# Kernel optimization log

Hardware: AMD Instinct MI355X
Metric: run time of the kernel (lower is better)

The kernel has to match this reference:

```python
import jax, jax.numpy as jnp
import numpy as np

N_NODES = 50000
N_EDGES = 800000
D_IN = 16


def gcn_conv(x, edge_index, W, b, n_nodes):
    """PyG GCNConv: x' = D^{-1/2} (A + I) D^{-1/2} X W + b (add_self_loops=True)."""
    h = x @ W  # [N, d_out] - transform before propagate (small d => cheaper)
    src = jnp.concatenate([edge_index[0], jnp.arange(n_nodes)])  # add self-loops
    dst = jnp.concatenate([edge_index[1], jnp.arange(n_nodes)])
    deg = jax.ops.segment_sum(jnp.ones_like(dst, dtype=h.dtype), dst,
                              num_segments=n_nodes)  # in-degree incl. self-loop
    deg_inv_sqrt = jnp.where(deg > 0, jax.lax.rsqrt(deg), 0.0)
    norm = deg_inv_sqrt[src] * deg_inv_sqrt[dst]  # [E+N]
    msg = h[src] * norm[:, None]                  # gather + scale
    out = jax.ops.segment_sum(msg, dst, num_segments=n_nodes)  # scatter-add
    return out + b


def setup_inputs() -> dict:
    key = jax.random.key(0)
    ks = jax.random.split(key, 16)
    d = D_IN
    x = jax.random.normal(ks[0], (N_NODES, d), dtype=jnp.float32)
    edge_index = jax.random.randint(ks[1], (2, N_EDGES), 0, N_NODES, dtype=jnp.int64)

    def glorot(k, fan_in, fan_out):
        s = (6.0 / (fan_in + fan_out)) ** 0.5
        return jax.random.uniform(k, (fan_in, fan_out), jnp.float32, -s, s)

    return {
        "x": x,
        "edge_index": edge_index,
        "W1": glorot(ks[2], d, 2 * d),      "b1": jnp.zeros((2 * d,), jnp.float32),
        "W2": glorot(ks[3], 2 * d, 4 * d),  "b2": jnp.zeros((4 * d,), jnp.float32),
        "W3": glorot(ks[4], 4 * d, 8 * d),  "b3": jnp.zeros((8 * d,), jnp.float32),
        "Wl1": glorot(ks[5], 8 * d, 4 * d), "bl1": jnp.zeros((4 * d,), jnp.float32),
        "Wl2": glorot(ks[6], 4 * d, 2 * d), "bl2": jnp.zeros((2 * d,), jnp.float32),
        "Wl3": glorot(ks[7], 2 * d, d),     "bl3": jnp.zeros((d,), jnp.float32),
    }


def reference(x, edge_index, W1, b1, W2, b2, W3, b3, Wl1, bl1, Wl2, bl2, Wl3, bl3):
    n = x.shape[0]
    # note: original applies relu twice per conv; relu is idempotent
    out = jax.nn.relu(gcn_conv(x, edge_index, W1, b1, n))
    out = jax.nn.relu(gcn_conv(out, edge_index, W2, b2, n))
    out = jax.nn.relu(gcn_conv(out, edge_index, W3, b3, n))
    out = jax.nn.relu(out @ Wl1 + bl1)
    out = jax.nn.relu(out @ Wl2 + bl2)
    out = jax.nn.relu(out @ Wl3 + bl3)
    return out
```

## Files before the change

kernel.cpp:

```cpp
#include <hip/hip_runtime.h>

#define TPB 256
#define TE  2048
#define MAXB 6144

typedef _Float16 half_t;
typedef _Float16 half4 __attribute__((ext_vector_type(4)));
typedef _Float16 half8 __attribute__((ext_vector_type(8)));
typedef float float8v __attribute__((ext_vector_type(8)));

static inline int cdiv(int a, int b) { return (a + b - 1) / b; }


__global__ void k_zero_int(int* p, int n) {
    int i = blockIdx.x * blockDim.x + threadIdx.x;
    if (i < n) p[i] = 0;
}

__global__ void __launch_bounds__(TPB)
k_binscatter(const int* __restrict__ src, const int* __restrict__ dst,
             int* __restrict__ bcur, unsigned int* __restrict__ gbuf,
             int e, int nb) {
    __shared__ int lcnt[256], loffs[256], lcur[256], gres[256];
    __shared__ int ss[256];
    __shared__ unsigned int ldata[TE];
    const int tid = threadIdx.x;
    const int base = blockIdx.x * TE;
    const int cnt = min(TE, e - base);
    lcnt[tid] = 0;
    __syncthreads();

    unsigned int myv[TE / TPB];
    int myb[TE / TPB];
#pragma unroll
    for (int k = 0; k < TE / TPB; ++k) {
        int j = tid + k * TPB;
        if (j < cnt) {
            int d = dst[base + j], s = src[base + j];
            int b = d >> 8;
            myv[k] = ((unsigned)b << 24) | ((unsigned)(d & 255) << 16) | (unsigned)s;
            myb[k] = b;
            atomicAdd(&lcnt[b], 1);
        } else myb[k] = -1;
    }
    __syncthreads();
    {
        int v = lcnt[tid];
        ss[tid] = v;
        __syncthreads();
        for (int d = 1; d < 256; d <<= 1) {
            int x2 = (tid >= d) ? ss[tid - d] : 0;
            __syncthreads();
            ss[tid] += x2;
            __syncthreads();
        }
        loffs[tid] = ss[tid] - v;
        lcur[tid] = ss[tid] - v;
    }
    __syncthreads();
    if (tid < nb && lcnt[tid])
        gres[tid] = tid * MAXB + atomicAdd(&bcur[tid], lcnt[tid]);
#pragma unroll
    for (int k = 0; k < TE / TPB; ++k) {
        if (myb[k] >= 0) {
            int p = atomicAdd(&lcur[myb[k]], 1);
            ldata[p] = myv[k];
        }
    }
    __syncthreads();
    for (int j = tid; j < cnt; j += TPB) {
        unsigned int v = ldata[j];
        int b = v >> 24;
        gbuf[gres[b] + (j - loffs[b])] = v & 0xFFFFFFu;
    }
}

__global__ void __launch_bounds__(TPB)
k_csr(const unsigned int* __restrict__ gbuf, const int* __restrict__ bcur,
      const float* __restrict__ x, int* __restrict__ offs,
      unsigned short* __restrict__ nch, float* __restrict__ dinv,
      unsigned short* __restrict__ ssrc, half_t* __restrict__ G, int n, int nb) {
    __shared__ int ss[256], cnt[256], loffs2[256], lcur2[256], pcnt[256];
    __shared__ float sdinv[256];
    __shared__ unsigned short stage[MAXB];
    const int b = blockIdx.x;
    const int t = threadIdx.x;
    const int s0 = b * MAXB;
    const int m = bcur[b];

    cnt[t] = 0;
    __syncthreads();
    for (int j = t; j < m; j += TPB)
        atomicAdd(&cnt[(gbuf[s0 + j] >> 16) & 255], 1);
    __syncthreads();
    {
        int v = cnt[t];
        int pv = (v + 7) & ~7;
        pcnt[t] = pv;
        ss[t] = pv;
        __syncthreads();
        for (int d = 1; d < 256; d <<= 1) {
            int x2 = (t >= d) ? ss[t - d] : 0;
            __syncthreads();
            ss[t] += x2;
            __syncthreads();
        }
        loffs2[t] = ss[t] - pv;
        lcur2[t] = ss[t] - pv;
        float di = rsqrtf((float)v + 1.0f);
        sdinv[t] = di;
        int node = b * 256 + t;
        if (node < n) {
            offs[node] = s0 + loffs2[t];
            nch[node] = (unsigned short)(pv >> 3);
            dinv[node] = di;
        }
    }
    __syncthreads();
    for (int j = t; j < m; j += TPB) {
        unsigned int v = gbuf[s0 + j];
        int p = atomicAdd(&lcur2[(v >> 16) & 255], 1);
        stage[p] = (unsigned short)(v & 0xFFFFu);
    }
    __syncthreads();
    {
        int base2 = loffs2[t] + cnt[t], end2 = loffs2[t] + pcnt[t];
        for (int q = base2; q < end2; ++q) stage[q] = (unsigned short)n;
    }
    __syncthreads();
    const int tot = ss[255];
    for (int j = t; j < tot; j += TPB) ssrc[s0 + j] = stage[j];

    const int base = b * 256;
    const int cn = min(256, n - base);
    const float4* X4 = (const float4*)x;
    half4* G4 = (half4*)G;
    for (int j = t; j < cn * 4; j += TPB) {
        int nl = j >> 2, k4 = j & 3;
        float4 v = X4[(size_t)(base + nl) * 4 + k4];
        float d = sdinv[nl];
        half4 h;
        h.x = (half_t)(v.x * d); h.y = (half_t)(v.y * d);
        h.z = (half_t)(v.z * d); h.w = (half_t)(v.w * d);
        G4[(size_t)(base + nl) * 4 + k4] = h;
    }
    if (b == 0 && t < 4) G4[(size_t)n * 4 + t] = half4{0, 0, 0, 0};
}

template<int DI, int DO, int R, bool SCALE, bool OUT_HALF, bool WHALF, bool ZSENT>
__global__ void __launch_bounds__(TPB, 4)
k_conv(const int* __restrict__ offs, const unsigned short* __restrict__ nch,
       const unsigned short* __restrict__ ssrc,
       const half_t* __restrict__ G, const float* __restrict__ dinv,
       const float* __restrict__ W, const float* __restrict__ b,
       void* __restrict__ outp, int n) {
    constexpr int CT = DO / 4;
    constexpr int RT = TPB / CT;
    constexpr int TM = RT * R;
    constexpr int K4 = DI / 4;
    constexpr int PX = K4 + 1;
    constexpr int C  = DI / 8;
    static_assert(TM * C == TPB, "gather/gemm tile mismatch");
    __shared__ float4 sW4[WHALF ? 1 : DI * CT];
    __shared__ half4  sWh[WHALF ? DI * CT : 1];
    __shared__ float4 sX4[TM * PX];
    __shared__ int soffs[TM];
    __shared__ unsigned short snch[TM];
    const int tid = threadIdx.x;
    const int r0 = blockIdx.x * TM;

    const float4* Wg = (const float4*)W;
    for (int t = tid; t < DI * CT; t += TPB) {
        float4 w = Wg[t];
        if (WHALF) {
            half4 h;
            h.x = (half_t)w.x; h.y = (half_t)w.y;
            h.z = (half_t)w.z; h.w = (half_t)w.w;
            sWh[t] = h;
        } else {
            sW4[t] = w;
        }
    }
    if (tid < TM) {
        int row = r0 + tid;
        soffs[tid] = (row < n) ? offs[row] : 0;
        snch[tid] = (row < n) ? nch[row] : (unsigned short)0;
    }
    __syncthreads();

    {
        int lrow = tid / C;
        int gc = tid - lrow * C;
        int row = r0 + lrow;
        float8v acc;
#pragma unroll
        for (int q = 0; q < 8; ++q) acc[q] = 0.f;
        if (row < n) {
            const half8* Grow = (const half8*)G;
            const unsigned gcU = (unsigned)gc;
            half8 hs = Grow[(unsigned)row * C + gcU];
#pragma unroll
            for (int q = 0; q < 8; ++q) acc[q] = (float)hs[q];
            const int nchunks = snch[lrow];
            const uint4* sv = (const uint4*)(ssrc + soffs[lrow]);
            int k = 0;
            for (; k + 2 <= nchunks; k += 2) {
                uint4 pa = sv[k];
                uint4 pb = sv[k + 1];
                unsigned a0 = pa.x & 0xFFFFu, a1 = pa.x >> 16;
                unsigned a2 = pa.y & 0xFFFFu, a3 = pa.y >> 16;
                unsigned a4 = pa.z & 0xFFFFu, a5 = pa.z >> 16;
                unsigned a6 = pa.w & 0xFFFFu, a7 = pa.w >> 16;
                unsigned b0 = pb.x & 0xFFFFu, b1 = pb.x >> 16;
                unsigned b2 = pb.y & 0xFFFFu, b3 = pb.y >> 16;
                unsigned b4 = pb.z & 0xFFFFu, b5 = pb.z >> 16;
                unsigned b6 = pb.w & 0xFFFFu, b7 = pb.w >> 16;
                half8 ga0 = Grow[a0 * C + gcU];
                half8 ga1 = Grow[a1 * C + gcU];
                half8 ga2 = Grow[a2 * C + gcU];
                half8 ga3 = Grow[a3 * C + gcU];
                half8 ga4 = Grow[a4 * C + gcU];
                half8 ga5 = Grow[a5 * C + gcU];
                half8 ga6 = Grow[a6 * C + gcU];
                half8 ga7 = Grow[a7 * C + gcU];
                half8 gb0 = Grow[b0 * C + gcU];
                half8 gb1 = Grow[b1 * C + gcU];
                half8 gb2 = Grow[b2 * C + gcU];
                half8 gb3 = Grow[b3 * C + gcU];
                half8 gb4 = Grow[b4 * C + gcU];
                half8 gb5 = Grow[b5 * C + gcU];
                half8 gb6 = Grow[b6 * C + gcU];
                half8 gb7 = Grow[b7 * C + gcU];
#pragma unroll
                for (int q = 0; q < 8; ++q)
                    acc[q] += (((((float)ga0[q] + (float)ga1[q]) + ((float)ga2[q] + (float)ga3[q]))
                             +  (((float)ga4[q] + (float)ga5[q]) + ((float)ga6[q] + (float)ga7[q])))
                             + ((((float)gb0[q] + (float)gb1[q]) + ((float)gb2[q] + (float)gb3[q]))
                             +  (((float)gb4[q] + (float)gb5[q]) + ((float)gb6[q] + (float)gb7[q]))));
            }
            if (k < nchunks) {
                uint4 pk = sv[k];
                unsigned a0 = pk.x & 0xFFFFu, a1 = pk.x >> 16;
                unsigned a2 = pk.y & 0xFFFFu, a3 = pk.y >> 16;
                unsigned a4 = pk.z & 0xFFFFu, a5 = pk.z >> 16;
                unsigned a6 = pk.w & 0xFFFFu, a7 = pk.w >> 16;
                half8 g0 = Grow[a0 * C + gcU];
                half8 g1 = Grow[a1 * C + gcU];
                half8 g2 = Grow[a2 * C + gcU];
                half8 g3 = Grow[a3 * C + gcU];
                half8 g4 = Grow[a4 * C + gcU];
                half8 g5 = Grow[a5 * C + gcU];
                half8 g6 = Grow[a6 * C + gcU];
                half8 g7 = Grow[a7 * C + gcU];
#pragma unroll
                for (int q = 0; q < 8; ++q)
                    acc[q] += (((float)g0[q] + (float)g1[q]) + ((float)g2[q] + (float)g3[q]))
                            + (((float)g4[q] + (float)g5[q]) + ((float)g6[q] + (float)g7[q]));
            }
            float di = dinv[row];
#pragma unroll
            for (int q = 0; q < 8; ++q) acc[q] *= di;
        }
        sX4[lrow * PX + 2 * gc]     = make_float4(acc[0], acc[1], acc[2], acc[3]);
        sX4[lrow * PX + 2 * gc + 1] = make_float4(acc[4], acc[5], acc[6], acc[7]);
    }
    __syncthreads();

    const int c = tid & (CT - 1);
    const int rg = tid / CT;
    const int rbase = rg * R;
    float4 acc[R];
#pragma unroll
    for (int r = 0; r < R; ++r) acc[r] = make_float4(0.f, 0.f, 0.f, 0.f);

#pragma unroll 2
    for (int k4 = 0; k4 < K4; ++k4) {
        float4 xv[R];
#pragma unroll
        for (int r = 0; r < R; ++r) xv[r] = sX4[(rbase + r) * PX + k4];
#pragma unroll
        for (int kk = 0; kk < 4; ++kk) {
            float4 wv;
            if (WHALF) {
                half4 wh = sWh[(k4 * 4 + kk) * CT + c];
                wv = make_float4((float)wh.x, (float)wh.y, (float)wh.z, (float)wh.w);
            } else {
                wv = sW4[(k4 * 4 + kk) * CT + c];
            }
#pragma unroll
            for (int r = 0; r < R; ++r) {
                float xs = (kk == 0) ? xv[r].x : (kk == 1) ? xv[r].y
                         : (kk == 2) ? xv[r].z : xv[r].w;
                acc[r].x += xs * wv.x; acc[r].y += xs * wv.y;
                acc[r].z += xs * wv.z; acc[r].w += xs * wv.w;
            }
        }
    }

    float4 bc = ((const float4*)b)[c];
#pragma unroll
    for (int r = 0; r < R; ++r) {
        int row = r0 + rbase + r;
        if (row < n) {
            float4 o;
            o.x = fmaxf(acc[r].x + bc.x, 0.f);
            o.y = fmaxf(acc[r].y + bc.y, 0.f);
            o.z = fmaxf(acc[r].z + bc.z, 0.f);
            o.w = fmaxf(acc[r].w + bc.w, 0.f);
            if (SCALE) {
                float d = dinv[row];
                o.x *= d; o.y *= d; o.z *= d; o.w *= d;
            }
            if (OUT_HALF) {
                half4 h;
                h.x = (half_t)o.x; h.y = (half_t)o.y;
                h.z = (half_t)o.z; h.w = (half_t)o.w;
                ((half4*)outp)[(size_t)row * CT + c] = h;
            } else {
                ((float4*)outp)[(size_t)row * CT + c] = o;
            }
        }
    }
    if (ZSENT && OUT_HALF && blockIdx.x == 0 && tid < CT)
        ((half4*)outp)[(size_t)n * CT + tid] = half4{0, 0, 0, 0};
}

__global__ void __launch_bounds__(256, 3)
k_head(const half_t* __restrict__ X,
       const float* __restrict__ W1, const float* __restrict__ b1,
       const float* __restrict__ W2, const float* __restrict__ b2,
       const float* __restrict__ W3, const float* __restrict__ b3,
       float* __restrict__ out, int n) {
    __shared__ half_t hW1[128 * 64];
    __shared__ half_t hW2[64 * 32];
    __shared__ half_t hW3[32 * 16];
    __shared__ float h1[64 * 65];
    __shared__ float h2[64 * 33];
    const int tid = threadIdx.x;
    const int r0 = blockIdx.x * 64;

    for (int t = tid; t < 128 * 64; t += 256) hW1[t] = (half_t)W1[t];
    for (int t = tid; t < 64 * 32; t += 256) hW2[t] = (half_t)W2[t];
    for (int t = tid; t < 32 * 16; t += 256) hW3[t] = (half_t)W3[t];
    __syncthreads();

    {
        const int c4 = tid & 15;
        const int rowg = tid >> 4;
        const half8* Xr = (const half8*)X;
        float acc[4][4];
#pragma unroll
        for (int r = 0; r < 4; ++r)
#pragma unroll
            for (int j = 0; j < 4; ++j) acc[r][j] = 0.f;
        for (int k8 = 0; k8 < 16; ++k8) {
            half8 xh[4];
#pragma unroll
            for (int r = 0; r < 4; ++r) {
                int row = r0 + rowg * 4 + r;
                if (row < n) xh[r] = Xr[(size_t)row * 16 + k8];
                else { half8 z; for (int q = 0; q < 8; ++q) z[q] = (half_t)0.f; xh[r] = z; }
            }
#pragma unroll
            for (int q = 0; q < 8; ++q) {
                int k = k8 * 8 + q;
                half4 w = *(const half4*)&hW1[k * 64 + c4 * 4];
                float w0 = (float)w.x, w1 = (float)w.y, w2 = (float)w.z, w3 = (float)w.w;
#pragma unroll
                for (int r = 0; r < 4; ++r) {
                    float xs = (float)xh[r][q];
                    acc[r][0] += xs * w0; acc[r][1] += xs * w1;
                    acc[r][2] += xs * w2; acc[r][3] += xs * w3;
                }
            }
        }
        float4 bc = ((const float4*)b1)[c4];
#pragma unroll
        for (int r = 0; r < 4; ++r) {
            int rl = rowg * 4 + r;
            h1[rl * 65 + c4 * 4 + 0] = fmaxf(acc[r][0] + bc.x, 0.f);
            h1[rl * 65 + c4 * 4 + 1] = fmaxf(acc[r][1] + bc.y, 0.f);
            h1[rl * 65 + c4 * 4 + 2] = fmaxf(acc[r][2] + bc.z, 0.f);
            h1[rl * 65 + c4 * 4 + 3] = fmaxf(acc[r][3] + bc.w, 0.f);
        }
    }
    __syncthreads();

    {
        const int c4 = tid & 7;
        const int rowg = tid >> 3;
        float acc[2][4];
#pragma unroll
        for (int r = 0; r < 2; ++r)
#pragma unroll
            for (int j = 0; j < 4; ++j) acc[r][j] = 0.f;
#pragma unroll 4
        for (int k = 0; k < 64; ++k) {
            half4 w = *(const half4*)&hW2[k * 32 + c4 * 4];
            float w0 = (float)w.x, w1 = (float)w.y, w2 = (float)w.z, w3 = (float)w.w;
#pragma unroll
            for (int r = 0; r < 2; ++r) {
                float xs = h1[(rowg * 2 + r) * 65 + k];
                acc[r][0] += xs * w0; acc[r][1] += xs * w1;
                acc[r][2] += xs * w2; acc[r][3] += xs * w3;
            }
        }
        float4 bc = ((const float4*)b2)[c4];
#pragma unroll
        for (int r = 0; r < 2; ++r) {
            int rl = rowg * 2 + r;
            h2[rl * 33 + c4 * 4 + 0] = fmaxf(acc[r][0] + bc.x, 0.f);
            h2[rl * 33 + c4 * 4 + 1] = fmaxf(acc[r][1] + bc.y, 0.f);
            h2[rl * 33 + c4 * 4 + 2] = fmaxf(acc[r][2] + bc.z, 0.f);
            h2[rl * 33 + c4 * 4 + 3] = fmaxf(acc[r][3] + bc.w, 0.f);
        }
    }
    __syncthreads();

    {
        const int c4 = tid & 3;
        const int rl = tid >> 2;
        float a0 = 0.f, a1 = 0.f, a2 = 0.f, a3 = 0.f;
#pragma unroll 4
        for (int k = 0; k < 32; ++k) {
            half4 w = *(const half4*)&hW3[k * 16 + c4 * 4];
            float xs = h2[rl * 33 + k];
            a0 += xs * (float)w.x; a1 += xs * (float)w.y;
            a2 += xs * (float)w.z; a3 += xs * (float)w.w;
        }
        int row = r0 + rl;
        if (row < n) {
            float4 bc = ((const float4*)b3)[c4];
            float4 o;
            o.x = fmaxf(a0 + bc.x, 0.f);
            o.y = fmaxf(a1 + bc.y, 0.f);
            o.z = fmaxf(a2 + bc.z, 0.f);
            o.w = fmaxf(a3 + bc.w, 0.f);
            ((float4*)out)[(size_t)row * 4 + c4] = o;
        }
    }
}

extern "C" void kernel_launch(void* const* d_in, const int* in_sizes, int n_in,
                              void* d_out, int out_size, void* d_ws, size_t ws_size,
                              hipStream_t stream) {
    const float* x   = (const float*)d_in[0];
    const int*   ei  = (const int*)d_in[1];
    const float* W1  = (const float*)d_in[2];
    const float* bb1 = (const float*)d_in[3];
    const float* W2  = (const float*)d_in[4];
    const float* bb2 = (const float*)d_in[5];
    const float* W3  = (const float*)d_in[6];
    const float* bb3 = (const float*)d_in[7];
    const float* Wl1 = (const float*)d_in[8];
    const float* bl1 = (const float*)d_in[9];
    const float* Wl2 = (const float*)d_in[10];
    const float* bl2 = (const float*)d_in[11];
    const float* Wl3 = (const float*)d_in[12];
    const float* bl3 = (const float*)d_in[13];
    float* out = (float*)d_out;

    const int n = in_sizes[0] / 16;
    const int e = in_sizes[1] / 2;
    const int* src = ei;
    const int* dst = ei + e;
    const int nb = cdiv(n, 256);

    char* p = (char*)d_ws;
    auto alloc = [&](size_t bytes) {
        char* r = p;
        p += (bytes + 255) & ~(size_t)255;
        return r;
    };
    float*          dinv = (float*)         alloc((size_t)n * 4);
    int*            offs = (int*)           alloc((size_t)n * 4);
    unsigned short* nch  = (unsigned short*)alloc((size_t)n * 2);
    int*            bcur = (int*)           alloc(256 * 4);
    unsigned int*   gbuf = (unsigned int*)  alloc((size_t)nb * MAXB * 4);
    unsigned short* ssrc = (unsigned short*)alloc((size_t)nb * MAXB * 2);
    half_t*         H1   = (half_t*)        alloc((size_t)(n + 1) * 64 * 2);
    half_t*         H2   = (half_t*)        alloc((size_t)(n + 1) * 32 * 2);
    half_t*         X3h  = (half_t*)        alloc((size_t)n * 128 * 2);

    k_zero_int<<<1, 256, 0, stream>>>(bcur, 256);
    k_binscatter<<<cdiv(e, TE), TPB, 0, stream>>>(src, dst, bcur, gbuf, e, nb);
    k_csr<<<nb, TPB, 0, stream>>>(gbuf, bcur, x, offs, nch, dinv, ssrc, H1, n, nb);

    k_conv<16, 32, 4, true, true, false, true><<<cdiv(n, 128), TPB, 0, stream>>>(
        offs, nch, ssrc, H1, dinv, W1, bb1, H2, n);
    k_conv<32, 64, 4, true, true, false, true><<<cdiv(n, 64), TPB, 0, stream>>>(
        offs, nch, ssrc, H2, dinv, W2, bb2, H1, n);
    k_conv<64, 128, 4, false, true, true, false><<<cdiv(n, 32), TPB, 0, stream>>>(
        offs, nch, ssrc, H1, dinv, W3, bb3, X3h, n);

    k_head<<<cdiv(n, 64), 256, 0, stream>>>(X3h, Wl1, bl1, Wl2, bl2, Wl3, bl3, out, n);
}
```

Baseline: 198.9 us.

## Fuse third GCN conv with MLP head and count node degrees during binning

The third graph convolution is merged with the three-layer MLP head into one kernel. The 128-wide hidden features now stay in shared memory, through a union that reuses the conv-stage buffers, so the fp16 X3 intermediate is no longer written to and read back from global memory. Per-node in-degrees are counted with global atomics in the binning kernel, which removes the counting pass over gbuf in the CSR kernel. A single memset replaces the zeroing kernel. In exchange, every edge now issues a global atomic, and the head converts Wl1 to fp16 in every 32-row block, which adds per-block weight-load overhead.

Result: slower. 218.2 us (+9.7%).

```diff
diff --git a/kernel.cpp b/kernel.cpp
--- a/kernel.cpp
+++ b/kernel.cpp
@@ -12,15 +12,10 @@
 static inline int cdiv(int a, int b) { return (a + b - 1) / b; }
 
 
-__global__ void k_zero_int(int* p, int n) {
-    int i = blockIdx.x * blockDim.x + threadIdx.x;
-    if (i < n) p[i] = 0;
-}
-
 __global__ void __launch_bounds__(TPB)
 k_binscatter(const int* __restrict__ src, const int* __restrict__ dst,
-             int* __restrict__ bcur, unsigned int* __restrict__ gbuf,
-             int e, int nb) {
+             int* __restrict__ bcur, int* __restrict__ ncnt,
+             unsigned int* __restrict__ gbuf, int e, int nb) {
     __shared__ int lcnt[256], loffs[256], lcur[256], gres[256];
     __shared__ int ss[256];
     __shared__ unsigned int ldata[TE];
@@ -41,6 +36,7 @@
             myv[k] = ((unsigned)b << 24) | ((unsigned)(d & 255) << 16) | (unsigned)s;
             myb[k] = b;
             atomicAdd(&lcnt[b], 1);
+            atomicAdd(&ncnt[d], 1);
         } else myb[k] = -1;
     }
     __syncthreads();
@@ -77,10 +73,11 @@
 
 __global__ void __launch_bounds__(TPB)
 k_csr(const unsigned int* __restrict__ gbuf, const int* __restrict__ bcur,
-      const float* __restrict__ x, int* __restrict__ offs,
-      unsigned short* __restrict__ nch, float* __restrict__ dinv,
-      unsigned short* __restrict__ ssrc, half_t* __restrict__ G, int n, int nb) {
-    __shared__ int ss[256], cnt[256], loffs2[256], lcur2[256], pcnt[256];
+      const int* __restrict__ ncnt, const float* __restrict__ x,
+      int* __restrict__ offs, unsigned short* __restrict__ nch,
+      float* __restrict__ dinv, unsigned short* __restrict__ ssrc,
+      half_t* __restrict__ G, int n, int nb) {
+    __shared__ int ss[256], lcur2[256];
     __shared__ float sdinv[256];
     __shared__ unsigned short stage[MAXB];
     const int b = blockIdx.x;
@@ -88,45 +85,35 @@
     const int s0 = b * MAXB;
     const int m = bcur[b];
 
-    cnt[t] = 0;
-    __syncthreads();
-    for (int j = t; j < m; j += TPB)
-        atomicAdd(&cnt[(gbuf[s0 + j] >> 16) & 255], 1);
-    __syncthreads();
-    {
-        int v = cnt[t];
-        int pv = (v + 7) & ~7;
-        pcnt[t] = pv;
-        ss[t] = pv;
+    const int v = ncnt[b * 256 + t];
+    const int pv = (v + 7) & ~7;
+    ss[t] = pv;
+    __syncthreads();
+    for (int d = 1; d < 256; d <<= 1) {
+        int x2 = (t >= d) ? ss[t - d] : 0;
         __syncthreads();
-        for (int d = 1; d < 256; d <<= 1) {
-            int x2 = (t >= d) ? ss[t - d] : 0;
-            __syncthreads();
-            ss[t] += x2;
-            __syncthreads();
-        }
-        loffs2[t] = ss[t] - pv;
-        lcur2[t] = ss[t] - pv;
-        float di = rsqrtf((float)v + 1.0f);
-        sdinv[t] = di;
-        int node = b * 256 + t;
-        if (node < n) {
-            offs[node] = s0 + loffs2[t];
-            nch[node] = (unsigned short)(pv >> 3);
-            dinv[node] = di;
-        }
+        ss[t] += x2;
+        __syncthreads();
+    }
+    const int lo = ss[t] - pv;
+    lcur2[t] = lo;
+    float di = rsqrtf((float)v + 1.0f);
+    sdinv[t] = di;
+    int node = b * 256 + t;
+    if (node < n) {
+        offs[node] = s0 + lo;
+        nch[node] = (unsigned short)(pv >> 3);
+        dinv[node] = di;
     }
     __syncthreads();
     for (int j = t; j < m; j += TPB) {
-        unsigned int v = gbuf[s0 + j];
-        int p = atomicAdd(&lcur2[(v >> 16) & 255], 1);
-        stage[p] = (unsigned short)(v & 0xFFFFu);
-    }
-    __syncthreads();
-    {
-        int base2 = loffs2[t] + cnt[t], end2 = loffs2[t] + pcnt[t];
-        for (int q = base2; q < end2; ++q) stage[q] = (unsigned short)n;
-    }
+        unsigned int u = gbuf[s0 + j];
+        int p = atomicAdd(&lcur2[(u >> 16) & 255], 1);
+        stage[p] = (unsigned short)(u & 0xFFFFu);
+    }
+    __syncthreads();
+    for (int q = lo + v; q < lo + pv; ++q)
+        stage[q] = (unsigned short)n;
     __syncthreads();
     const int tot = ss[255];
     for (int j = t; j < tot; j += TPB) ssrc[s0 + j] = stage[j];
@@ -137,11 +124,11 @@
     half4* G4 = (half4*)G;
     for (int j = t; j < cn * 4; j += TPB) {
         int nl = j >> 2, k4 = j & 3;
-        float4 v = X4[(size_t)(base + nl) * 4 + k4];
+        float4 vv = X4[(size_t)(base + nl) * 4 + k4];
         float d = sdinv[nl];
         half4 h;
-        h.x = (half_t)(v.x * d); h.y = (half_t)(v.y * d);
-        h.z = (half_t)(v.z * d); h.w = (half_t)(v.w * d);
+        h.x = (half_t)(vv.x * d); h.y = (half_t)(vv.y * d);
+        h.z = (half_t)(vv.z * d); h.w = (half_t)(vv.w * d);
         G4[(size_t)(base + nl) * 4 + k4] = h;
     }
     if (b == 0 && t < 4) G4[(size_t)n * 4 + t] = half4{0, 0, 0, 0};
@@ -272,7 +259,6 @@
     float4 acc[R];
 #pragma unroll
     for (int r = 0; r < R; ++r) acc[r] = make_float4(0.f, 0.f, 0.f, 0.f);
-
 #pragma unroll 2
     for (int k4 = 0; k4 < K4; ++k4) {
         float4 xv[R];
@@ -325,118 +311,250 @@
         ((half4*)outp)[(size_t)n * CT + tid] = half4{0, 0, 0, 0};
 }
 
-__global__ void __launch_bounds__(256, 3)
-k_head(const half_t* __restrict__ X,
-       const float* __restrict__ W1, const float* __restrict__ b1,
-       const float* __restrict__ W2, const float* __restrict__ b2,
-       const float* __restrict__ W3, const float* __restrict__ b3,
-       float* __restrict__ out, int n) {
-    __shared__ half_t hW1[128 * 64];
-    __shared__ half_t hW2[64 * 32];
-    __shared__ half_t hW3[32 * 16];
-    __shared__ float h1[64 * 65];
-    __shared__ float h2[64 * 33];
+__global__ void __launch_bounds__(TPB, 4)
+k_conv3_head(const int* __restrict__ offs, const unsigned short* __restrict__ nch,
+             const unsigned short* __restrict__ ssrc,
+             const half_t* __restrict__ G, const float* __restrict__ dinv,
+             const float* __restrict__ W, const float* __restrict__ b,
+             const float* __restrict__ Wl1, const float* __restrict__ bl1,
+             const float* __restrict__ Wl2, const float* __restrict__ bl2,
+             const float* __restrict__ Wl3, const float* __restrict__ bl3,
+             float* __restrict__ out, int n) {
+    constexpr int DI = 64, DO = 128, R = 4;
+    constexpr int CT = DO / 4;
+    constexpr int TM = (TPB / CT) * R;
+    constexpr int K4 = DI / 4;
+    constexpr int PX = K4 + 1;
+    constexpr int C  = DI / 8;
+    constexpr int XP = 136;
+    __shared__ union {
+        struct { half4 sWh[DI * CT]; float4 sX4[TM * PX]; } g;
+        struct { half_t X3[TM * XP]; half_t hW1[128 * 64];
+                 float h1[TM * 65]; float h2[TM * 33]; } h;
+    } S;
+    __shared__ int soffs[TM];
+    __shared__ unsigned short snch[TM];
     const int tid = threadIdx.x;
-    const int r0 = blockIdx.x * 64;
-
-    for (int t = tid; t < 128 * 64; t += 256) hW1[t] = (half_t)W1[t];
-    for (int t = tid; t < 64 * 32; t += 256) hW2[t] = (half_t)W2[t];
-    for (int t = tid; t < 32 * 16; t += 256) hW3[t] = (half_t)W3[t];
+    const int r0 = blockIdx.x * TM;
+
+    const float4* Wg = (const float4*)W;
+    for (int t = tid; t < DI * CT; t += TPB) {
+        float4 w = Wg[t];
+        half4 hh;
+        hh.x = (half_t)w.x; hh.y = (half_t)w.y;
+        hh.z = (half_t)w.z; hh.w = (half_t)w.w;
+        S.g.sWh[t] = hh;
+    }
+    if (tid < TM) {
+        int row = r0 + tid;
+        soffs[tid] = (row < n) ? offs[row] : 0;
+        snch[tid] = (row < n) ? nch[row] : (unsigned short)0;
+    }
+    __syncthreads();
+
+    {
+        int lrow = tid / C;
+        int gc = tid - lrow * C;
+        int row = r0 + lrow;
+        float8v acc;
+#pragma unroll
+        for (int q = 0; q < 8; ++q) acc[q] = 0.f;
+        if (row < n) {
+            const half8* Grow = (const half8*)G;
+            const unsigned gcU = (unsigned)gc;
+            half8 hs = Grow[(unsigned)row * C + gcU];
+#pragma unroll
+            for (int q = 0; q < 8; ++q) acc[q] = (float)hs[q];
+            const int nchunks = snch[lrow];
+            const uint4* sv = (const uint4*)(ssrc + soffs[lrow]);
+            int k = 0;
+            for (; k + 2 <= nchunks; k += 2) {
+                uint4 pa = sv[k];
+                uint4 pb = sv[k + 1];
+                unsigned a0 = pa.x & 0xFFFFu, a1 = pa.x >> 16;
+                unsigned a2 = pa.y & 0xFFFFu, a3 = pa.y >> 16;
+                unsigned a4 = pa.z & 0xFFFFu, a5 = pa.z >> 16;
+                unsigned a6 = pa.w & 0xFFFFu, a7 = pa.w >> 16;
+                unsigned b0 = pb.x & 0xFFFFu, b1 = pb.x >> 16;
+                unsigned b2 = pb.y & 0xFFFFu, b3 = pb.y >> 16;
+                unsigned b4 = pb.z & 0xFFFFu, b5 = pb.z >> 16;
+                unsigned b6 = pb.w & 0xFFFFu, b7 = pb.w >> 16;
+                half8 ga0 = Grow[a0 * C + gcU];
+                half8 ga1 = Grow[a1 * C + gcU];
+                half8 ga2 = Grow[a2 * C + gcU];
+                half8 ga3 = Grow[a3 * C + gcU];
+                half8 ga4 = Grow[a4 * C + gcU];
+                half8 ga5 = Grow[a5 * C + gcU];
+                half8 ga6 = Grow[a6 * C + gcU];
+                half8 ga7 = Grow[a7 * C + gcU];
+                half8 gb0 = Grow[b0 * C + gcU];
+                half8 gb1 = Grow[b1 * C + gcU];
+                half8 gb2 = Grow[b2 * C + gcU];
+                half8 gb3 = Grow[b3 * C + gcU];
+                half8 gb4 = Grow[b4 * C + gcU];
+                half8 gb5 = Grow[b5 * C + gcU];
+                half8 gb6 = Grow[b6 * C + gcU];
+                half8 gb7 = Grow[b7 * C + gcU];
+#pragma unroll
+                for (int q = 0; q < 8; ++q)
+                    acc[q] += (((((float)ga0[q] + (float)ga1[q]) + ((float)ga2[q] + (float)ga3[q]))
+                             +  (((float)ga4[q] + (float)ga5[q]) + ((float)ga6[q] + (float)ga7[q])))
+                             + ((((float)gb0[q] + (float)gb1[q]) + ((float)gb2[q] + (float)gb3[q]))
+                             +  (((float)gb4[q] + (float)gb5[q]) + ((float)gb6[q] + (float)gb7[q]))));
+            }
+            if (k < nchunks) {
+                uint4 pk = sv[k];
+                unsigned a0 = pk.x & 0xFFFFu, a1 = pk.x >> 16;
+                unsigned a2 = pk.y & 0xFFFFu, a3 = pk.y >> 16;
+                unsigned a4 = pk.z & 0xFFFFu, a5 = pk.z >> 16;
+                unsigned a6 = pk.w & 0xFFFFu, a7 = pk.w >> 16;
+                half8 g0 = Grow[a0 * C + gcU];
+                half8 g1 = Grow[a1 * C + gcU];
+                half8 g2 = Grow[a2 * C + gcU];
+                half8 g3 = Grow[a3 * C + gcU];
+                half8 g4 = Grow[a4 * C + gcU];
+                half8 g5 = Grow[a5 * C + gcU];
+                half8 g6 = Grow[a6 * C + gcU];
+                half8 g7 = Grow[a7 * C + gcU];
+#pragma unroll
+                for (int q = 0; q < 8; ++q)
+                    acc[q] += (((float)g0[q] + (float)g1[q]) + ((float)g2[q] + (float)g3[q]))
+                            + (((float)g4[q] + (float)g5[q]) + ((float)g6[q] + (float)g7[q]));
+            }
+            float di = dinv[row];
+#pragma unroll
+            for (int q = 0; q < 8; ++q) acc[q] *= di;
+        }
+        S.g.sX4[lrow * PX + 2 * gc]     = make_float4(acc[0], acc[1], acc[2], acc[3]);
+        S.g.sX4[lrow * PX + 2 * gc + 1] = make_float4(acc[4], acc[5], acc[6], acc[7]);
+    }
+    __syncthreads();
+
+    const int c = tid & (CT - 1);
+    const int rg = tid / CT;
+    const int rbase = rg * R;
+    float4 acc[R];
+#pragma unroll
+    for (int r = 0; r < R; ++r) acc[r] = make_float4(0.f, 0.f, 0.f, 0.f);
+#pragma unroll 2
+    for (int k4 = 0; k4 < K4; ++k4) {
+        float4 xv[R];
+#pragma unroll
+        for (int r = 0; r < R; ++r) xv[r] = S.g.sX4[(rbase + r) * PX + k4];
+#pragma unroll
+        for (int kk = 0; kk < 4; ++kk) {
+            half4 wh = S.g.sWh[(k4 * 4 + kk) * CT + c];
+            float4 wv = make_float4((float)wh.x, (float)wh.y, (float)wh.z, (float)wh.w);
+#pragma unroll
+            for (int r = 0; r < R; ++r) {
+                float xs = (kk == 0) ? xv[r].x : (kk == 1) ? xv[r].y
+                         : (kk == 2) ? xv[r].z : xv[r].w;
+                acc[r].x += xs * wv.x; acc[r].y += xs * wv.y;
+                acc[r].z += xs * wv.z; acc[r].w += xs * wv.w;
+            }
+        }
+    }
+    {
+        float4 bc = ((const float4*)b)[c];
+#pragma unroll
+        for (int r = 0; r < R; ++r) {
+            acc[r].x = fmaxf(acc[r].x + bc.x, 0.f);
+            acc[r].y = fmaxf(acc[r].y + bc.y, 0.f);
+            acc[r].z = fmaxf(acc[r].z + bc.z, 0.f);
+            acc[r].w = fmaxf(acc[r].w + bc.w, 0.f);
+        }
+    }
+    __syncthreads();
+
+#pragma unroll
+    for (int r = 0; r < R; ++r) {
+        half4 hv;
+        hv.x = (half_t)acc[r].x; hv.y = (half_t)acc[r].y;
+        hv.z = (half_t)acc[r].z; hv.w = (half_t)acc[r].w;
+        *(half4*)&S.h.X3[(rbase + r) * XP + c * 4] = hv;
+    }
+    for (int t = tid; t < 128 * 64; t += TPB) S.h.hW1[t] = (half_t)Wl1[t];
     __syncthreads();
 
     {
         const int c4 = tid & 15;
         const int rowg = tid >> 4;
-        const half8* Xr = (const half8*)X;
-        float acc[4][4];
-#pragma unroll
-        for (int r = 0; r < 4; ++r)
-#pragma unroll
-            for (int j = 0; j < 4; ++j) acc[r][j] = 0.f;
+        float a1[2][4];
+#pragma unroll
+        for (int r = 0; r < 2; ++r)
+#pragma unroll
+            for (int j = 0; j < 4; ++j) a1[r][j] = 0.f;
         for (int k8 = 0; k8 < 16; ++k8) {
-            half8 xh[4];
-#pragma unroll
-            for (int r = 0; r < 4; ++r) {
-                int row = r0 + rowg * 4 + r;
-                if (row < n) xh[r] = Xr[(size_t)row * 16 + k8];
-                else { half8 z; for (int q = 0; q < 8; ++q) z[q] = (half_t)0.f; xh[r] = z; }
-            }
+            half8 xh[2];
+#pragma unroll
+            for (int r = 0; r < 2; ++r)
+                xh[r] = *(const half8*)&S.h.X3[(rowg * 2 + r) * XP + k8 * 8];
 #pragma unroll
             for (int q = 0; q < 8; ++q) {
                 int k = k8 * 8 + q;
-                half4 w = *(const half4*)&hW1[k * 64 + c4 * 4];
+                half4 w = *(const half4*)&S.h.hW1[k * 64 + c4 * 4];
                 float w0 = (float)w.x, w1 = (float)w.y, w2 = (float)w.z, w3 = (float)w.w;
 #pragma unroll
-                for (int r = 0; r < 4; ++r) {
+                for (int r = 0; r < 2; ++r) {
                     float xs = (float)xh[r][q];
-                    acc[r][0] += xs * w0; acc[r][1] += xs * w1;
-                    acc[r][2] += xs * w2; acc[r][3] += xs * w3;
+                    a1[r][0] += xs * w0; a1[r][1] += xs * w1;
+                    a1[r][2] += xs * w2; a1[r][3] += xs * w3;
                 }
             }
         }
-        float4 bc = ((const float4*)b1)[c4];
-#pragma unroll
-        for (int r = 0; r < 4; ++r) {
-            int rl = rowg * 4 + r;
-            h1[rl * 65 + c4 * 4 + 0] = fmaxf(acc[r][0] + bc.x, 0.f);
-            h1[rl * 65 + c4 * 4 + 1] = fmaxf(acc[r][1] + bc.y, 0.f);
-            h1[rl * 65 + c4 * 4 + 2] = fmaxf(acc[r][2] + bc.z, 0.f);
-            h1[rl * 65 + c4 * 4 + 3] = fmaxf(acc[r][3] + bc.w, 0.f);
+        float4 bc = ((const float4*)bl1)[c4];
+#pragma unroll
+        for (int r = 0; r < 2; ++r) {
+            int rl = rowg * 2 + r;
+            S.h.h1[rl * 65 + c4 * 4 + 0] = fmaxf(a1[r][0] + bc.x, 0.f);
+            S.h.h1[rl * 65 + c4 * 4 + 1] = fmaxf(a1[r][1] + bc.y, 0.f);
+            S.h.h1[rl * 65 + c4 * 4 + 2] = fmaxf(a1[r][2] + bc.z, 0.f);
+            S.h.h1[rl * 65 + c4 * 4 + 3] = fmaxf(a1[r][3] + bc.w, 0.f);
         }
     }
     __syncthreads();
 
     {
         const int c4 = tid & 7;
-        const int rowg = tid >> 3;
-        float acc[2][4];
-#pragma unroll
-        for (int r = 0; r < 2; ++r)
-#pragma unroll
-            for (int j = 0; j < 4; ++j) acc[r][j] = 0.f;
+        const int rl = tid >> 3;
+        float a2[4] = {0.f, 0.f, 0.f, 0.f};
 #pragma unroll 4
         for (int k = 0; k < 64; ++k) {
-            half4 w = *(const half4*)&hW2[k * 32 + c4 * 4];
-            float w0 = (float)w.x, w1 = (float)w.y, w2 = (float)w.z, w3 = (float)w.w;
-#pragma unroll
-            for (int r = 0; r < 2; ++r) {
-                float xs = h1[(rowg * 2 + r) * 65 + k];
-                acc[r][0] += xs * w0; acc[r][1] += xs * w1;
-                acc[r][2] += xs * w2; acc[r][3] += xs * w3;
-            }
-        }
-        float4 bc = ((const float4*)b2)[c4];
-#pragma unroll
-        for (int r = 0; r < 2; ++r) {
-            int rl = rowg * 2 + r;
-            h2[rl * 33 + c4 * 4 + 0] = fmaxf(acc[r][0] + bc.x, 0.f);
-            h2[rl * 33 + c4 * 4 + 1] = fmaxf(acc[r][1] + bc.y, 0.f);
-            h2[rl * 33 + c4 * 4 + 2] = fmaxf(acc[r][2] + bc.z, 0.f);
-            h2[rl * 33 + c4 * 4 + 3] = fmaxf(acc[r][3] + bc.w, 0.f);
-        }
+            float4 w = ((const float4*)Wl2)[k * 8 + c4];
+            float xs = S.h.h1[rl * 65 + k];
+            a2[0] += xs * w.x; a2[1] += xs * w.y;
+            a2[2] += xs * w.z; a2[3] += xs * w.w;
+        }
+        float4 bc = ((const float4*)bl2)[c4];
+        S.h.h2[rl * 33 + c4 * 4 + 0] = fmaxf(a2[0] + bc.x, 0.f);
+        S.h.h2[rl * 33 + c4 * 4 + 1] = fmaxf(a2[1] + bc.y, 0.f);
+        S.h.h2[rl * 33 + c4 * 4 + 2] = fmaxf(a2[2] + bc.z, 0.f);
+        S.h.h2[rl * 33 + c4 * 4 + 3] = fmaxf(a2[3] + bc.w, 0.f);
     }
     __syncthreads();
 
     {
         const int c4 = tid & 3;
         const int rl = tid >> 2;
-        float a0 = 0.f, a1 = 0.f, a2 = 0.f, a3 = 0.f;
+        if (rl < TM) {
+            float s0 = 0.f, s1 = 0.f, s2 = 0.f, s3 = 0.f;
 #pragma unroll 4
-        for (int k = 0; k < 32; ++k) {
-            half4 w = *(const half4*)&hW3[k * 16 + c4 * 4];
-            float xs = h2[rl * 33 + k];
-            a0 += xs * (float)w.x; a1 += xs * (float)w.y;
-            a2 += xs * (float)w.z; a3 += xs * (float)w.w;
-        }
-        int row = r0 + rl;
-        if (row < n) {
-            float4 bc = ((const float4*)b3)[c4];
-            float4 o;
-            o.x = fmaxf(a0 + bc.x, 0.f);
-            o.y = fmaxf(a1 + bc.y, 0.f);
-            o.z = fmaxf(a2 + bc.z, 0.f);
-            o.w = fmaxf(a3 + bc.w, 0.f);
-            ((float4*)out)[(size_t)row * 4 + c4] = o;
+            for (int k = 0; k < 32; ++k) {
+                float4 w = ((const float4*)Wl3)[k * 4 + c4];
+                float xs = S.h.h2[rl * 33 + k];
+                s0 += xs * w.x; s1 += xs * w.y;
+                s2 += xs * w.z; s3 += xs * w.w;
+            }
+            int row = r0 + rl;
+            if (row < n) {
+                float4 bc = ((const float4*)bl3)[c4];
+                float4 o;
+                o.x = fmaxf(s0 + bc.x, 0.f);
+                o.y = fmaxf(s1 + bc.y, 0.f);
+                o.z = fmaxf(s2 + bc.z, 0.f);
+                o.w = fmaxf(s3 + bc.w, 0.f);
+                ((float4*)out)[(size_t)row * 4 + c4] = o;
+            }
         }
     }
 }
@@ -472,26 +590,24 @@
         p += (bytes + 255) & ~(size_t)255;
         return r;
     };
+    int*            bcur = (int*)           alloc(1024);
+    int*            ncnt = (int*)           alloc((size_t)nb * 256 * 4);
     float*          dinv = (float*)         alloc((size_t)n * 4);
     int*            offs = (int*)           alloc((size_t)n * 4);
     unsigned short* nch  = (unsigned short*)alloc((size_t)n * 2);
-    int*            bcur = (int*)           alloc(256 * 4);
     unsigned int*   gbuf = (unsigned int*)  alloc((size_t)nb * MAXB * 4);
     unsigned short* ssrc = (unsigned short*)alloc((size_t)nb * MAXB * 2);
     half_t*         H1   = (half_t*)        alloc((size_t)(n + 1) * 64 * 2);
     half_t*         H2   = (half_t*)        alloc((size_t)(n + 1) * 32 * 2);
-    half_t*         X3h  = (half_t*)        alloc((size_t)n * 128 * 2);
-
-    k_zero_int<<<1, 256, 0, stream>>>(bcur, 256);
-    k_binscatter<<<cdiv(e, TE), TPB, 0, stream>>>(src, dst, bcur, gbuf, e, nb);
-    k_csr<<<nb, TPB, 0, stream>>>(gbuf, bcur, x, offs, nch, dinv, ssrc, H1, n, nb);
+
+    hipMemsetAsync(bcur, 0, 1024 + (size_t)nb * 256 * 4, stream);
+    k_binscatter<<<cdiv(e, TE), TPB, 0, stream>>>(src, dst, bcur, ncnt, gbuf, e, nb);
+    k_csr<<<nb, TPB, 0, stream>>>(gbuf, bcur, ncnt, x, offs, nch, dinv, ssrc, H1, n, nb);
 
     k_conv<16, 32, 4, true, true, false, true><<<cdiv(n, 128), TPB, 0, stream>>>(
         offs, nch, ssrc, H1, dinv, W1, bb1, H2, n);
     k_conv<32, 64, 4, true, true, false, true><<<cdiv(n, 64), TPB, 0, stream>>>(
         offs, nch, ssrc, H2, dinv, W2, bb2, H1, n);
-    k_conv<64, 128, 4, false, true, true, false><<<cdiv(n, 32), TPB, 0, stream>>>(
-        offs, nch, ssrc, H1, dinv, W3, bb3, X3h, n);
-
-    k_head<<<cdiv(n, 64), 256, 0, stream>>>(X3h, Wl1, bl1, Wl2, bl2, Wl3, bl3, out, n);
+    k_conv3_head<<<cdiv(n, 32), TPB, 0, stream>>>(
+        offs, nch, ssrc, H1, dinv, W3, bb3, Wl1, bl1, Wl2, bl2, Wl3, bl3, out, n);
 }
```
